# Optimization experiments

Hardware: AMD Instinct MI355X
Metric: run time of the kernel (lower is better)

The kernel has to match this reference:

```python
import jax, jax.numpy as jnp
import numpy as np


def _rev_excl_cumsum(x):
    # sum over j > i along leading axis: reverse inclusive cumsum minus self
    return jnp.flip(jnp.cumsum(jnp.flip(x, 0), 0), 0) - x


def setup_inputs() -> dict:
    key = jax.random.key(0)
    k1, k2, k3, k4, k5 = jax.random.split(key, 5)
    T1, B, M = 4095, 64, 128  # t-1 existing stack entries, batch, embed dim
    V = jax.random.normal(k1, (T1, B, M), dtype=jnp.float32)
    s = jax.random.uniform(k2, (T1, B, 1), dtype=jnp.float32)
    d = jax.random.uniform(k3, (B, 1), dtype=jnp.float32)
    u = jax.random.uniform(k4, (B, 1), dtype=jnp.float32)
    v = jax.random.normal(k5, (B, M), dtype=jnp.float32)
    return {"V": V, "s": s, "d": d, "u": u, "v": v}


def reference(V, s, d, u, v):
    # V: [t-1, B, M], s: [t-1, B, 1], d,u: [B,1], v: [B,M]
    # Push v onto the stack
    Vn = jnp.concatenate([V, v[None]], axis=0)            # [t, B, M]
    # New strengths: sn[i] = relu(s[i] - relu(u - sum_{j>i} s[j])), sn[t-1] = d
    totprev = _rev_excl_cumsum(s)                          # [t-1, B, 1]
    sn_head = jax.nn.relu(s - jax.nn.relu(u[None] - totprev))
    sn = jnp.concatenate([sn_head, d[None]], axis=0)       # [t, B, 1]
    # Readout: r = sum_i min(sn[i], relu(1 - sum_{j>i} sn[j])) * Vn[i]
    tots = _rev_excl_cumsum(sn)                            # [t, B, 1]
    coeff = jnp.minimum(sn, jax.nn.relu(1.0 - tots))       # [t, B, 1]
    r = jnp.sum(coeff * Vn, axis=0)                        # [B, M]
    return Vn, sn, r
```

## Files before the change

### kernel.cpp

```cpp
#include <hip/hip_runtime.h>
#include <hip/hip_bf16.h>

#define T1 4095
#define TT 4096
#define B  64
#define M  128
#define BM (B * M)
#define ROW4 (BM / 4)
#define SCAN_THREADS 1024
#define NWAVE (SCAN_THREADS / 64)
#define EPT (TT / SCAN_THREADS)
#define IPB 32
#define HPB (IPB / 2)
#define NCHUNK (TT / IPB)

typedef float f32x4 __attribute__((ext_vector_type(4)));

__global__ __launch_bounds__(SCAN_THREADS) void scan_kernel(
    const float* __restrict__ s,
    const float* __restrict__ d,
    const float* __restrict__ u,
    float* __restrict__ snT,
    float* __restrict__ coeffT)
{
    const int b = blockIdx.x;
    const int t = threadIdx.x;
    const int lane = t & 63;
    const int wave = t >> 6;
    __shared__ float wtot1[NWAVE];
    __shared__ float wtot2[NWAVE];

    const int base = t * EPT;
    float sv[EPT];
    float sum = 0.f;
#pragma unroll
    for (int k = 0; k < EPT; ++k) {
        int i = base + k;
        float val = (i < T1) ? s[(size_t)i * B + b] : 0.f;
        sv[k] = val;
        sum += val;
    }

    float x = sum;
#pragma unroll
    for (int off = 1; off < 64; off <<= 1) {
        float y = __shfl_down(x, off);
        if (lane + off < 64) x += y;
    }
    if (lane == 0) wtot1[wave] = x;
    __syncthreads();
    float after = 0.f;
#pragma unroll
    for (int w = 0; w < NWAVE; ++w)
        if (w > wave) after += wtot1[w];
    float suffix = after + x - sum;

    const float ub = u[b];
    float tot = suffix;
    float snv[EPT];
#pragma unroll
    for (int k = EPT - 1; k >= 0; --k) {
        float sval = sv[k];
        snv[k] = fmaxf(sval - fmaxf(ub - tot, 0.f), 0.f);
        tot += sval;
    }
    if (t == SCAN_THREADS - 1) snv[EPT - 1] = d[b];

    float sum2 = 0.f;
#pragma unroll
    for (int k = 0; k < EPT; ++k) sum2 += snv[k];
    float x2 = sum2;
#pragma unroll
    for (int off = 1; off < 64; off <<= 1) {
        float y = __shfl_down(x2, off);
        if (lane + off < 64) x2 += y;
    }
    if (lane == 0) wtot2[wave] = x2;
    __syncthreads();
    float after2 = 0.f;
#pragma unroll
    for (int w = 0; w < NWAVE; ++w)
        if (w > wave) after2 += wtot2[w];
    float suffix2 = after2 + x2 - sum2;

    float tot2 = suffix2;
    float cv[EPT];
#pragma unroll
    for (int k = EPT - 1; k >= 0; --k) {
        float snval = snv[k];
        cv[k] = fminf(snval, fmaxf(1.f - tot2, 0.f));
        tot2 += snval;
    }
    f32x4 sv4 = { snv[0], snv[1], snv[2], snv[3] };
    *(f32x4*)(snT + (size_t)b * TT + base) = sv4;
    f32x4 cc = { cv[0], cv[1], cv[2], cv[3] };
    *(f32x4*)(coeffT + (size_t)b * TT + base) = cc;
}

__global__ __launch_bounds__(512) void fuse_kernel(
    const float* __restrict__ V,
    const float* __restrict__ v,
    const float* __restrict__ coeffT,
    float* __restrict__ Vn,
    float* __restrict__ partials)
{
    const int bmTile = blockIdx.x;
    const int chunk  = blockIdx.y;
    const int tid  = threadIdx.x;
    const int half = tid >> 8;
    const int t    = tid & 255;
    const int bm4  = bmTile * 256 + t;
    const int b    = bm4 >> 5;
    const int i0   = chunk * IPB + half * HPB;

    float c[HPB];
    const f32x4* cp = (const f32x4*)(coeffT + (size_t)b * TT + i0);
#pragma unroll
    for (int q = 0; q < HPB / 4; ++q) {
        f32x4 cc = cp[q];
        c[4*q+0] = cc.x; c[4*q+1] = cc.y; c[4*q+2] = cc.z; c[4*q+3] = cc.w;
    }

    f32x4 acc = {0.f, 0.f, 0.f, 0.f};
    const f32x4* Vp  = (const f32x4*)V;
    f32x4*       Vnp = (f32x4*)Vn;

    const bool lastHalf = (chunk == NCHUNK - 1) && (half == 1);
    if (!lastHalf) {
#pragma unroll
        for (int k = 0; k < HPB; ++k) {
            const size_t idx = (size_t)(i0 + k) * ROW4 + bm4;
            f32x4 val = Vp[idx];
            __builtin_nontemporal_store(val, &Vnp[idx]);
            acc += c[k] * val;
        }
    } else {
#pragma unroll
        for (int k = 0; k < HPB - 1; ++k) {
            const size_t idx = (size_t)(i0 + k) * ROW4 + bm4;
            f32x4 val = Vp[idx];
            __builtin_nontemporal_store(val, &Vnp[idx]);
            acc += c[k] * val;
        }
        f32x4 val = ((const f32x4*)v)[bm4];
        __builtin_nontemporal_store(val, &Vnp[(size_t)T1 * ROW4 + bm4]);
        acc += c[HPB - 1] * val;
    }

    __shared__ f32x4 sh[256];
    if (half == 1) sh[t] = acc;
    __syncthreads();
    if (half == 0)
        ((f32x4*)partials)[(size_t)chunk * ROW4 + bm4] = acc + sh[t];
}

__global__ __launch_bounds__(256) void finish_kernel(
    const float* __restrict__ partials,
    const float* __restrict__ snT,
    float* __restrict__ r,
    float* __restrict__ sn_out)
{
    const int blk = blockIdx.x;
    const int tid = threadIdx.x;

    if (blk < 64) {
        const int grp = tid >> 5;
        const int lane = tid & 31;
        const int out4 = blk * 32 + lane;

        f32x4 acc = {0.f, 0.f, 0.f, 0.f};
#pragma unroll 8
        for (int c = grp; c < NCHUNK; c += 8)
            acc += ((const f32x4*)partials)[(size_t)c * ROW4 + out4];

        __shared__ f32x4 sh[256];
        sh[tid] = acc;
        __syncthreads();
        if (tid < 128) sh[tid] += sh[tid + 128];
        __syncthreads();
        if (tid < 64) sh[tid] += sh[tid + 64];
        __syncthreads();
        if (tid < 32) {
            f32x4 res = sh[tid] + sh[tid + 32];
            ((f32x4*)r)[out4] = res;
        }
    } else {
        const int g = blk - 64;
        __shared__ float tile[64][65];

        const int b  = tid >> 2;
        const int iq = tid & 3;
        const f32x4* src4 = (const f32x4*)(snT + (size_t)b * TT + g * 64 + iq * 16);
#pragma unroll
        for (int q = 0; q < 4; ++q) {
            f32x4 vv = src4[q];
            tile[iq * 16 + q * 4 + 0][b] = vv.x;
            tile[iq * 16 + q * 4 + 1][b] = vv.y;
            tile[iq * 16 + q * 4 + 2][b] = vv.z;
            tile[iq * 16 + q * 4 + 3][b] = vv.w;
        }
        __syncthreads();

        const int il = tid >> 6;
        const int bb = tid & 63;
#pragma unroll
        for (int p = 0; p < 16; ++p) {
            const int i = p * 4 + il;
            sn_out[(size_t)(g * 64 + i) * B + bb] = tile[i][bb];
        }
    }
}

extern "C" void kernel_launch(void* const* d_in, const int* in_sizes, int n_in,
                              void* d_out, int out_size, void* d_ws, size_t ws_size,
                              hipStream_t stream) {
    const float* V = (const float*)d_in[0];
    const float* s = (const float*)d_in[1];
    const float* d = (const float*)d_in[2];
    const float* u = (const float*)d_in[3];
    const float* v = (const float*)d_in[4];

    float* out = (float*)d_out;
    float* Vn = out;
    float* sn = out + (size_t)TT * BM;
    float* r  = sn + (size_t)TT * B;

    float* coeffT   = (float*)d_ws;
    float* snT      = coeffT + (size_t)B * TT;
    float* partials = snT + (size_t)B * TT;

    scan_kernel<<<B, SCAN_THREADS, 0, stream>>>(s, d, u, snT, coeffT);
    fuse_kernel<<<dim3(8, NCHUNK), 512, 0, stream>>>(V, v, coeffT, Vn, partials);
    finish_kernel<<<128, 256, 0, stream>>>(partials, snT, r, sn);
}
```

Baseline: 56.41 us.

## Fuse scan, fuse and finish stages into one cooperative kernel with grid syncs

Replaces the three kernel launches with a single cooperative kernel of 256 blocks. The kernel runs the per-batch scan, then the V copy plus weighted accumulation with four chunks per block, then the partial reduction and sn transpose, separated by grid-wide syncs. The goal is to remove launch gaps and inter-kernel drain. The trade-off is much lower parallelism in the bandwidth-bound copy stage (256 blocks instead of 1024) and the cost of the grid barriers. The three-kernel path stays as a fallback, and per-call device attribute and occupancy queries add host overhead.

```diff
diff --git a/kernel.cpp b/kernel.cpp
--- a/kernel.cpp
+++ b/kernel.cpp
@@ -1,5 +1,8 @@
 #include <hip/hip_runtime.h>
 #include <hip/hip_bf16.h>
+#include <hip/hip_cooperative_groups.h>
+
+namespace cg = cooperative_groups;
 
 #define T1 4095
 #define TT 4096
@@ -7,40 +10,239 @@
 #define M  128
 #define BM (B * M)
 #define ROW4 (BM / 4)
-#define SCAN_THREADS 1024
-#define NWAVE (SCAN_THREADS / 64)
-#define EPT (TT / SCAN_THREADS)
 #define IPB 32
 #define HPB (IPB / 2)
 #define NCHUNK (TT / IPB)
 
+#define MT 512
+#define MWAVES (MT / 64)
+#define MSEPT (TT / MT)
+#define MGRID 256
+#define MCPB 4
+
+#define FST 1024
+#define FNW (FST / 64)
+#define FEPT (TT / FST)
+
 typedef float f32x4 __attribute__((ext_vector_type(4)));
 
-__global__ __launch_bounds__(SCAN_THREADS) void scan_kernel(
+__global__ __launch_bounds__(MT) void mega_kernel(
+    const float* __restrict__ V,
     const float* __restrict__ s,
     const float* __restrict__ d,
     const float* __restrict__ u,
+    const float* __restrict__ v,
+    float* __restrict__ Vn,
+    float* __restrict__ sn_out,
+    float* __restrict__ r,
+    float* __restrict__ coeffT,
     float* __restrict__ snT,
-    float* __restrict__ coeffT)
+    float* __restrict__ partials)
+{
+    cg::grid_group grid = cg::this_grid();
+    const int bid = blockIdx.x;
+    const int tid = threadIdx.x;
+
+    __shared__ __align__(16) char smem[64 * 65 * 4];
+    __shared__ float wtot1[MWAVES], wtot2[MWAVES];
+
+    if (bid < B) {
+        const int b = bid;
+        const int lane = tid & 63, wave = tid >> 6;
+        const int base = tid * MSEPT;
+
+        float sv[MSEPT];
+        float sum = 0.f;
+#pragma unroll
+        for (int k = 0; k < MSEPT; ++k) {
+            int i = base + k;
+            float val = (i < T1) ? s[(size_t)i * B + b] : 0.f;
+            sv[k] = val;
+            sum += val;
+        }
+        float x = sum;
+#pragma unroll
+        for (int off = 1; off < 64; off <<= 1) {
+            float y = __shfl_down(x, off);
+            if (lane + off < 64) x += y;
+        }
+        if (lane == 0) wtot1[wave] = x;
+        __syncthreads();
+        float after = 0.f;
+#pragma unroll
+        for (int w = 0; w < MWAVES; ++w)
+            if (w > wave) after += wtot1[w];
+        float suffix = after + x - sum;
+
+        const float ub = u[b];
+        float tot = suffix;
+        float snv[MSEPT];
+#pragma unroll
+        for (int k = MSEPT - 1; k >= 0; --k) {
+            float sval = sv[k];
+            snv[k] = fmaxf(sval - fmaxf(ub - tot, 0.f), 0.f);
+            tot += sval;
+        }
+        if (tid == MT - 1) snv[MSEPT - 1] = d[b];
+
+        float sum2 = 0.f;
+#pragma unroll
+        for (int k = 0; k < MSEPT; ++k) sum2 += snv[k];
+        float x2 = sum2;
+#pragma unroll
+        for (int off = 1; off < 64; off <<= 1) {
+            float y = __shfl_down(x2, off);
+            if (lane + off < 64) x2 += y;
+        }
+        if (lane == 0) wtot2[wave] = x2;
+        __syncthreads();
+        float after2 = 0.f;
+#pragma unroll
+        for (int w = 0; w < MWAVES; ++w)
+            if (w > wave) after2 += wtot2[w];
+        float suffix2 = after2 + x2 - sum2;
+
+        float tot2 = suffix2;
+        float cv[MSEPT];
+#pragma unroll
+        for (int k = MSEPT - 1; k >= 0; --k) {
+            float snval = snv[k];
+            cv[k] = fminf(snval, fmaxf(1.f - tot2, 0.f));
+            tot2 += snval;
+        }
+        f32x4* sp = (f32x4*)(snT + (size_t)b * TT + base);
+        sp[0] = (f32x4){snv[0], snv[1], snv[2], snv[3]};
+        sp[1] = (f32x4){snv[4], snv[5], snv[6], snv[7]};
+        f32x4* cp = (f32x4*)(coeffT + (size_t)b * TT + base);
+        cp[0] = (f32x4){cv[0], cv[1], cv[2], cv[3]};
+        cp[1] = (f32x4){cv[4], cv[5], cv[6], cv[7]};
+    }
+
+    grid.sync();
+
+    {
+        const int bmTile = bid & 7;
+        const int cg0 = bid >> 3;
+        const int half = tid >> 8;
+        const int t = tid & 255;
+        const int bm4 = bmTile * 256 + t;
+        const int b = bm4 >> 5;
+        f32x4* shc = (f32x4*)smem;
+        const f32x4* Vp  = (const f32x4*)V;
+        f32x4*       Vnp = (f32x4*)Vn;
+        const float* cbase = coeffT + (size_t)b * TT;
+
+#pragma unroll
+        for (int cc = 0; cc < MCPB; ++cc) {
+            const int chunk = cg0 + cc * 32;
+            const int i0 = chunk * IPB + half * HPB;
+
+            float c[HPB];
+            const f32x4* cp = (const f32x4*)(cbase + i0);
+#pragma unroll
+            for (int q = 0; q < HPB / 4; ++q) {
+                f32x4 cv4 = cp[q];
+                c[4*q+0] = cv4.x; c[4*q+1] = cv4.y; c[4*q+2] = cv4.z; c[4*q+3] = cv4.w;
+            }
+
+            f32x4 acc = {0.f, 0.f, 0.f, 0.f};
+            const bool lastHalf = (chunk == NCHUNK - 1) && (half == 1);
+            if (!lastHalf) {
+#pragma unroll
+                for (int k = 0; k < HPB; ++k) {
+                    const size_t idx = (size_t)(i0 + k) * ROW4 + bm4;
+                    f32x4 val = Vp[idx];
+                    __builtin_nontemporal_store(val, &Vnp[idx]);
+                    acc += c[k] * val;
+                }
+            } else {
+#pragma unroll
+                for (int k = 0; k < HPB - 1; ++k) {
+                    const size_t idx = (size_t)(i0 + k) * ROW4 + bm4;
+                    f32x4 val = Vp[idx];
+                    __builtin_nontemporal_store(val, &Vnp[idx]);
+                    acc += c[k] * val;
+                }
+                f32x4 val = ((const f32x4*)v)[bm4];
+                __builtin_nontemporal_store(val, &Vnp[(size_t)T1 * ROW4 + bm4]);
+                acc += c[HPB - 1] * val;
+            }
+
+            __syncthreads();
+            if (half == 1) shc[t] = acc;
+            __syncthreads();
+            if (half == 0)
+                ((f32x4*)partials)[(size_t)chunk * ROW4 + bm4] = acc + shc[t];
+        }
+    }
+
+    grid.sync();
+
+    if (bid < 64) {
+        f32x4* sh512 = (f32x4*)smem;
+        const int grp = tid >> 5;
+        const int lane = tid & 31;
+        const int out4 = bid * 32 + lane;
+        f32x4 acc = {0.f, 0.f, 0.f, 0.f};
+#pragma unroll
+        for (int c = grp; c < NCHUNK; c += 16)
+            acc += ((const f32x4*)partials)[(size_t)c * ROW4 + out4];
+        sh512[tid] = acc;
+        __syncthreads();
+        if (tid < 256) sh512[tid] += sh512[tid + 256];
+        __syncthreads();
+        if (tid < 128) sh512[tid] += sh512[tid + 128];
+        __syncthreads();
+        if (tid < 64) sh512[tid] += sh512[tid + 64];
+        __syncthreads();
+        if (tid < 32) ((f32x4*)r)[out4] = sh512[tid] + sh512[tid + 32];
+    } else if (bid < 128) {
+        const int g = bid - 64;
+        float (*tile)[65] = (float(*)[65])smem;
+        {
+            const int b    = tid >> 3;
+            const int ioff = (tid & 7) * 8;
+            const f32x4* src4 = (const f32x4*)(snT + (size_t)b * TT + g * 64 + ioff);
+            f32x4 v0 = src4[0], v1 = src4[1];
+            tile[ioff+0][b] = v0.x; tile[ioff+1][b] = v0.y;
+            tile[ioff+2][b] = v0.z; tile[ioff+3][b] = v0.w;
+            tile[ioff+4][b] = v1.x; tile[ioff+5][b] = v1.y;
+            tile[ioff+6][b] = v1.z; tile[ioff+7][b] = v1.w;
+        }
+        __syncthreads();
+        {
+            const int i    = tid >> 3;
+            const int boff = (tid & 7) * 8;
+            float* dst = sn_out + (size_t)(g * 64 + i) * B + boff;
+            *(f32x4*)dst = (f32x4){tile[i][boff+0], tile[i][boff+1],
+                                   tile[i][boff+2], tile[i][boff+3]};
+            *(f32x4*)(dst + 4) = (f32x4){tile[i][boff+4], tile[i][boff+5],
+                                         tile[i][boff+6], tile[i][boff+7]};
+        }
+    }
+}
+
+__global__ __launch_bounds__(FST) void scan_kernel(
+    const float* __restrict__ s, const float* __restrict__ d,
+    const float* __restrict__ u,
+    float* __restrict__ snT, float* __restrict__ coeffT)
 {
     const int b = blockIdx.x;
     const int t = threadIdx.x;
     const int lane = t & 63;
     const int wave = t >> 6;
-    __shared__ float wtot1[NWAVE];
-    __shared__ float wtot2[NWAVE];
-
-    const int base = t * EPT;
-    float sv[EPT];
+    __shared__ float wtot1[FNW], wtot2[FNW];
+
+    const int base = t * FEPT;
+    float sv[FEPT];
     float sum = 0.f;
 #pragma unroll
-    for (int k = 0; k < EPT; ++k) {
+    for (int k = 0; k < FEPT; ++k) {
         int i = base + k;
         float val = (i < T1) ? s[(size_t)i * B + b] : 0.f;
         sv[k] = val;
         sum += val;
     }
-
     float x = sum;
 #pragma unroll
     for (int off = 1; off < 64; off <<= 1) {
@@ -51,24 +253,24 @@
     __syncthreads();
     float after = 0.f;
 #pragma unroll
-    for (int w = 0; w < NWAVE; ++w)
+    for (int w = 0; w < FNW; ++w)
         if (w > wave) after += wtot1[w];
     float suffix = after + x - sum;
 
     const float ub = u[b];
     float tot = suffix;
-    float snv[EPT];
-#pragma unroll
-    for (int k = EPT - 1; k >= 0; --k) {
+    float snv[FEPT];
+#pragma unroll
+    for (int k = FEPT - 1; k >= 0; --k) {
         float sval = sv[k];
         snv[k] = fmaxf(sval - fmaxf(ub - tot, 0.f), 0.f);
         tot += sval;
     }
-    if (t == SCAN_THREADS - 1) snv[EPT - 1] = d[b];
+    if (t == FST - 1) snv[FEPT - 1] = d[b];
 
     float sum2 = 0.f;
 #pragma unroll
-    for (int k = 0; k < EPT; ++k) sum2 += snv[k];
+    for (int k = 0; k < FEPT; ++k) sum2 += snv[k];
     float x2 = sum2;
 #pragma unroll
     for (int off = 1; off < 64; off <<= 1) {
@@ -79,30 +281,26 @@
     __syncthreads();
     float after2 = 0.f;
 #pragma unroll
-    for (int w = 0; w < NWAVE; ++w)
+    for (int w = 0; w < FNW; ++w)
         if (w > wave) after2 += wtot2[w];
     float suffix2 = after2 + x2 - sum2;
 
     float tot2 = suffix2;
-    float cv[EPT];
-#pragma unroll
-    for (int k = EPT - 1; k >= 0; --k) {
+    float cv[FEPT];
+#pragma unroll
+    for (int k = FEPT - 1; k >= 0; --k) {
         float snval = snv[k];
         cv[k] = fminf(snval, fmaxf(1.f - tot2, 0.f));
         tot2 += snval;
     }
-    f32x4 sv4 = { snv[0], snv[1], snv[2], snv[3] };
-    *(f32x4*)(snT + (size_t)b * TT + base) = sv4;
-    f32x4 cc = { cv[0], cv[1], cv[2], cv[3] };
-    *(f32x4*)(coeffT + (size_t)b * TT + base) = cc;
+    *(f32x4*)(snT + (size_t)b * TT + base) = (f32x4){snv[0], snv[1], snv[2], snv[3]};
+    *(f32x4*)(coeffT + (size_t)b * TT + base) = (f32x4){cv[0], cv[1], cv[2], cv[3]};
 }
 
 __global__ __launch_bounds__(512) void fuse_kernel(
-    const float* __restrict__ V,
-    const float* __restrict__ v,
+    const float* __restrict__ V, const float* __restrict__ v,
     const float* __restrict__ coeffT,
-    float* __restrict__ Vn,
-    float* __restrict__ partials)
+    float* __restrict__ Vn, float* __restrict__ partials)
 {
     const int bmTile = blockIdx.x;
     const int chunk  = blockIdx.y;
@@ -155,10 +353,8 @@
 }
 
 __global__ __launch_bounds__(256) void finish_kernel(
-    const float* __restrict__ partials,
-    const float* __restrict__ snT,
-    float* __restrict__ r,
-    float* __restrict__ sn_out)
+    const float* __restrict__ partials, const float* __restrict__ snT,
+    float* __restrict__ r, float* __restrict__ sn_out)
 {
     const int blk = blockIdx.x;
     const int tid = threadIdx.x;
@@ -180,10 +376,7 @@
         __syncthreads();
         if (tid < 64) sh[tid] += sh[tid + 64];
         __syncthreads();
-        if (tid < 32) {
-            f32x4 res = sh[tid] + sh[tid + 32];
-            ((f32x4*)r)[out4] = res;
-        }
+        if (tid < 32) ((f32x4*)r)[out4] = sh[tid] + sh[tid + 32];
     } else {
         const int g = blk - 64;
         __shared__ float tile[64][65];
@@ -229,7 +422,32 @@
     float* snT      = coeffT + (size_t)B * TT;
     float* partials = snT + (size_t)B * TT;
 
-    scan_kernel<<<B, SCAN_THREADS, 0, stream>>>(s, d, u, snT, coeffT);
-    fuse_kernel<<<dim3(8, NCHUNK), 512, 0, stream>>>(V, v, coeffT, Vn, partials);
-    finish_kernel<<<128, 256, 0, stream>>>(partials, snT, r, sn);
+    int dev = 0;
+    (void)hipGetDevice(&dev);
+    int coopOK = 0;
+    (void)hipDeviceGetAttribute(&coopOK, hipDeviceAttributeCooperativeLaunch, dev);
+    int numCU = 0;
+    (void)hipDeviceGetAttribute(&numCU, hipDeviceAttributeMultiprocessorCount, dev);
+    int maxBpc = 0;
+    hipError_t qe = hipOccupancyMaxActiveBlocksPerMultiprocessor(
+        &maxBpc, (const void*)mega_kernel, MT, 0);
+
+    bool done = false;
+    if (coopOK && qe == hipSuccess && (long)maxBpc * numCU >= MGRID) {
+        void* args[] = {
+            (void*)&V, (void*)&s, (void*)&d, (void*)&u, (void*)&v,
+            (void*)&Vn, (void*)&sn, (void*)&r,
+            (void*)&coeffT, (void*)&snT, (void*)&partials
+        };
+        hipError_t e = hipLaunchCooperativeKernel((const void*)mega_kernel,
+                                                  dim3(MGRID), dim3(MT),
+                                                  args, 0, stream);
+        if (e == hipSuccess) done = true;
+        else (void)hipGetLastError();
+    }
+    if (!done) {
+        scan_kernel<<<B, FST, 0, stream>>>(s, d, u, snT, coeffT);
+        fuse_kernel<<<dim3(8, NCHUNK), 512, 0, stream>>>(V, v, coeffT, Vn, partials);
+        finish_kernel<<<128, 256, 0, stream>>>(partials, snT, r, sn);
+    }
 }
```

After: 132.3 us. 135% more time.
